# Performance work log

Hardware: AMD Instinct MI355X
Metric: run time of the kernel (lower is better)

The kernel has to match this reference:

```python
import jax, jax.numpy as jnp
import numpy as np

VOCAB, D = 5, 64


def setup_inputs() -> dict:
    key = jax.random.key(0)
    ks = jax.random.split(key, 8)
    B, S = 8, 2048
    x = jax.random.randint(ks[0], (B, S), 0, VOCAB)
    emb_table = jax.random.normal(ks[1], (VOCAB, D), dtype=jnp.float32)
    wq = jax.random.normal(ks[2], (D, D), dtype=jnp.float32) * 0.1
    bq = jax.random.normal(ks[3], (D,), dtype=jnp.float32) * 0.1
    wk = jax.random.normal(ks[4], (D, D), dtype=jnp.float32) * 0.1
    bk = jax.random.normal(ks[5], (D,), dtype=jnp.float32) * 0.1
    wv = jax.random.normal(ks[6], (D, D), dtype=jnp.float32) * 0.1
    bv = jax.random.normal(ks[7], (D,), dtype=jnp.float32) * 0.1
    return {"x": x, "emb_table": emb_table, "wq": wq, "bq": bq,
            "wk": wk, "bk": bk, "wv": wv, "bv": bv}


def reference(x, emb_table, wq, bq, wk, bk, wv, bv):
    # Embedding lookup: [B, S, D]
    emb = emb_table[x]
    # torch Linear: y = x @ W.T + b
    Q = emb @ wq.T + bq
    K = emb @ wk.T + bk
    V = emb @ wv.T + bv
    scale = 1.0 / np.sqrt(D).astype(np.float32)
    # [B, S, S] attention scores
    scores = jnp.einsum('bqd,bkd->bqk', Q, K) * scale
    S_len = x.shape[-1]
    # causal mask: -inf strictly above the diagonal
    causal = jnp.tril(jnp.ones((S_len, S_len), dtype=bool))
    scores = jnp.where(causal, scores, jnp.float32(-jnp.inf))
    probs = jax.nn.softmax(scores, axis=-1)
    return jnp.einsum('bqk,bkd->bqd', probs, V)
```

## Files before the change

### kernel.cpp

```cpp
#include <hip/hip_runtime.h>
#include <math.h>

#define VOCAB 5
#define DIM   64
#define BATCH 8
#define SLEN  2048
#define SEG   64
#define SEGS_PER_B (SLEN / SEG)
#define BLOCK 256
#define WPAD  65

__global__ __launch_bounds__(BLOCK) void decoder_fused(
    const int* __restrict__ x, const float* __restrict__ emb,
    const float* __restrict__ wq, const float* __restrict__ bq,
    const float* __restrict__ wk, const float* __restrict__ bk,
    const float* __restrict__ wv, const float* __restrict__ bv,
    float* __restrict__ out)
{
    const int bid  = blockIdx.x;
    const int b    = bid >> 5;
    const int seg  = bid & 31;
    const int s0   = seg * SEG;
    const int t    = threadIdx.x;
    const int lane = t & 63;
    const int wave = t >> 6;

    __shared__ float wSh[3][DIM * WPAD];
    __shared__ float eSh[VOCAB * DIM];
    __shared__ float qSh[VOCAB * DIM];
    __shared__ float kSh[VOCAB * DIM];
    __shared__ __align__(16) float vSh[VOCAB * DIM];
    __shared__ float StabSh[VOCAB * VOCAB];
    __shared__ float ESh[VOCAB * VOCAB];
    __shared__ float pSh[SEG * VOCAB];
    __shared__ int   waveCnt[4][VOCAB];

    {
        const float4* wq4 = (const float4*)wq;
        const float4* wk4 = (const float4*)wk;
        const float4* wv4 = (const float4*)wv;
        for (int j = t; j < DIM * DIM / 4; j += BLOCK) {
            int d = j >> 4, i4 = (j & 15) << 2;
            float4 a = wq4[j], c = wk4[j], e = wv4[j];
            float* dq = &wSh[0][d * WPAD + i4];
            float* dk = &wSh[1][d * WPAD + i4];
            float* dv = &wSh[2][d * WPAD + i4];
            dq[0]=a.x; dq[1]=a.y; dq[2]=a.z; dq[3]=a.w;
            dk[0]=c.x; dk[1]=c.y; dk[2]=c.z; dk[3]=c.w;
            dv[0]=e.x; dv[1]=e.y; dv[2]=e.z; dv[3]=e.w;
        }
        for (int i = t; i < VOCAB * DIM; i += BLOCK) eSh[i] = emb[i];
    }
    __syncthreads();

    for (int idx = t; idx < VOCAB * DIM; idx += BLOCK) {
        int v = idx >> 6, d = idx & 63;
        float aq = bq[d], ak = bk[d], av = bv[d];
        const float* e  = &eSh[v * DIM];
        const float* rq = &wSh[0][d * WPAD];
        const float* rk = &wSh[1][d * WPAD];
        const float* rv = &wSh[2][d * WPAD];
        #pragma unroll 16
        for (int i = 0; i < DIM; ++i) {
            float ei = e[i];
            aq += ei * rq[i];
            ak += ei * rk[i];
            av += ei * rv[i];
        }
        qSh[idx] = aq; kSh[idx] = ak; vSh[idx] = av;
    }
    __syncthreads();

    if (t < VOCAB * VOCAB) {
        int i = t / VOCAB, j = t % VOCAB;
        float s = 0.f;
        #pragma unroll
        for (int d = 0; d < DIM; ++d) s += qSh[i * DIM + d] * kSh[j * DIM + d];
        StabSh[t] = s * 0.125f;
    }
    __syncthreads();
    if (t < VOCAB * VOCAB) {
        int row = t / VOCAB;
        float mx = StabSh[row * VOCAB];
        #pragma unroll
        for (int j = 1; j < VOCAB; ++j) mx = fmaxf(mx, StabSh[row * VOCAB + j]);
        ESh[t] = expf(StabSh[t] - mx);
    }

    const int* xb = x + b * SLEN;
    int base[VOCAB] = {0,0,0,0,0};
    const int nchunk = s0 >> 6;
    for (int c = wave; c < nchunk; c += 4) {
        int tk = xb[(c << 6) + lane];
        #pragma unroll
        for (int v = 0; v < VOCAB; ++v)
            base[v] += __popcll(__ballot(tk == v));
    }
    if (lane == 0) {
        #pragma unroll
        for (int v = 0; v < VOCAB; ++v) waveCnt[wave][v] = base[v];
    }
    const int tok = xb[s0 + lane];
    const unsigned long long leMask = (2ull << lane) - 1ull;
    int inc[VOCAB];
    #pragma unroll
    for (int v = 0; v < VOCAB; ++v)
        inc[v] = __popcll(__ballot(tok == v) & leMask);
    __syncthreads();

    if (t < SEG) {
        float wgt[VOCAB];
        float den = 0.f;
        #pragma unroll
        for (int v = 0; v < VOCAB; ++v) {
            int c = inc[v] + waveCnt[0][v] + waveCnt[1][v] + waveCnt[2][v] + waveCnt[3][v];
            float wv = (float)c * ESh[tok * VOCAB + v];
            wgt[v] = wv;
            den += wv;
        }
        float invd = 1.0f / den;
        #pragma unroll
        for (int v = 0; v < VOCAB; ++v) pSh[t * VOCAB + v] = wgt[v] * invd;
    }
    __syncthreads();

    const float4* Vs4 = reinterpret_cast<const float4*>(vSh);
    float4* out4 = reinterpret_cast<float4*>(out) + ((size_t)b * SLEN + s0) * (DIM / 4);
    for (int i = t; i < SEG * (DIM / 4); i += BLOCK) {
        int q = i >> 4, d4 = i & 15;
        float4 acc = make_float4(0.f, 0.f, 0.f, 0.f);
        #pragma unroll
        for (int v = 0; v < VOCAB; ++v) {
            float pw = pSh[q * VOCAB + v];
            float4 vv = Vs4[v * (DIM / 4) + d4];
            acc.x += pw * vv.x;
            acc.y += pw * vv.y;
            acc.z += pw * vv.z;
            acc.w += pw * vv.w;
        }
        out4[i] = acc;
    }
}

extern "C" void kernel_launch(void* const* d_in, const int* in_sizes, int n_in,
                              void* d_out, int out_size, void* d_ws, size_t ws_size,
                              hipStream_t stream) {
    const int*   x   = (const int*)d_in[0];
    const float* emb = (const float*)d_in[1];
    const float* wq  = (const float*)d_in[2];
    const float* bq  = (const float*)d_in[3];
    const float* wk  = (const float*)d_in[4];
    const float* bk  = (const float*)d_in[5];
    const float* wv  = (const float*)d_in[6];
    const float* bv  = (const float*)d_in[7];
    float* out = (float*)d_out;

    decoder_fused<<<BATCH * SEGS_PER_B, BLOCK, 0, stream>>>(
        x, emb, wq, bq, wk, bk, wv, bv, out);
}
```

Measured before the change: 12.34 us.

## Split block into weight-loading and token-counting wave groups, doubling block size

Doubles the block to 512 threads so four waves stage the Q/K/V weights into shared memory while the other four load embeddings and compute the prefix token counts at the same time, instead of doing both one after the other. The Q/K/V projection is mapped one wave per vocab row, and q/k rows are padded to avoid bank conflicts. The separate exp-table pass and one barrier are removed by folding the softmax exponentials into the per-token weight computation on the last wave. Larger blocks may lower occupancy, and several waves sit idle in later phases.

```diff
diff --git a/kernel.cpp b/kernel.cpp
--- a/kernel.cpp
+++ b/kernel.cpp
@@ -7,7 +7,7 @@
 #define SLEN  2048
 #define SEG   64
 #define SEGS_PER_B (SLEN / SEG)
-#define BLOCK 256
+#define BLOCK 512
 #define WPAD  65
 
 __global__ __launch_bounds__(BLOCK) void decoder_fused(
@@ -27,34 +27,68 @@
 
     __shared__ float wSh[3][DIM * WPAD];
     __shared__ float eSh[VOCAB * DIM];
-    __shared__ float qSh[VOCAB * DIM];
-    __shared__ float kSh[VOCAB * DIM];
+    __shared__ float qSh[VOCAB * WPAD];
+    __shared__ float kSh[VOCAB * WPAD];
     __shared__ __align__(16) float vSh[VOCAB * DIM];
     __shared__ float StabSh[VOCAB * VOCAB];
-    __shared__ float ESh[VOCAB * VOCAB];
     __shared__ float pSh[SEG * VOCAB];
-    __shared__ int   waveCnt[4][VOCAB];
+    __shared__ int   wcSh[4][VOCAB];
 
-    {
+    const int* xb = x + b * SLEN;
+
+    int tok = 0;
+    int inc[VOCAB] = {0, 0, 0, 0, 0};
+
+    if (wave < 4) {
         const float4* wq4 = (const float4*)wq;
         const float4* wk4 = (const float4*)wk;
         const float4* wv4 = (const float4*)wv;
-        for (int j = t; j < DIM * DIM / 4; j += BLOCK) {
+        for (int j = t; j < DIM * DIM / 4; j += 256) {
             int d = j >> 4, i4 = (j & 15) << 2;
-            float4 a = wq4[j], c = wk4[j], e = wv4[j];
-            float* dq = &wSh[0][d * WPAD + i4];
-            float* dk = &wSh[1][d * WPAD + i4];
-            float* dv = &wSh[2][d * WPAD + i4];
-            dq[0]=a.x; dq[1]=a.y; dq[2]=a.z; dq[3]=a.w;
-            dk[0]=c.x; dk[1]=c.y; dk[2]=c.z; dk[3]=c.w;
-            dv[0]=e.x; dv[1]=e.y; dv[2]=e.z; dv[3]=e.w;
+            float4 a = wq4[j];
+            float* dst = &wSh[0][d * WPAD + i4];
+            dst[0] = a.x; dst[1] = a.y; dst[2] = a.z; dst[3] = a.w;
         }
-        for (int i = t; i < VOCAB * DIM; i += BLOCK) eSh[i] = emb[i];
+        for (int j = t; j < DIM * DIM / 4; j += 256) {
+            int d = j >> 4, i4 = (j & 15) << 2;
+            float4 a = wk4[j];
+            float* dst = &wSh[1][d * WPAD + i4];
+            dst[0] = a.x; dst[1] = a.y; dst[2] = a.z; dst[3] = a.w;
+        }
+        for (int j = t; j < DIM * DIM / 4; j += 256) {
+            int d = j >> 4, i4 = (j & 15) << 2;
+            float4 a = wv4[j];
+            float* dst = &wSh[2][d * WPAD + i4];
+            dst[0] = a.x; dst[1] = a.y; dst[2] = a.z; dst[3] = a.w;
+        }
+    } else {
+        for (int i = t - 256; i < VOCAB * DIM; i += 256) eSh[i] = emb[i];
+
+        const int pw = wave - 4;
+        int base[VOCAB] = {0, 0, 0, 0, 0};
+        const int nchunk = s0 >> 6;
+        for (int c = pw; c < nchunk; c += 4) {
+            int tk = xb[(c << 6) + lane];
+            #pragma unroll
+            for (int v = 0; v < VOCAB; ++v)
+                base[v] += __popcll(__ballot(tk == v));
+        }
+        if (lane == 0) {
+            #pragma unroll
+            for (int v = 0; v < VOCAB; ++v) wcSh[pw][v] = base[v];
+        }
+        if (wave == 7) {
+            tok = xb[s0 + lane];
+            const unsigned long long leMask = (2ull << lane) - 1ull;
+            #pragma unroll
+            for (int v = 0; v < VOCAB; ++v)
+                inc[v] = __popcll(__ballot(tok == v) & leMask);
+        }
     }
     __syncthreads();
 
-    for (int idx = t; idx < VOCAB * DIM; idx += BLOCK) {
-        int v = idx >> 6, d = idx & 63;
+    if (wave < 5) {
+        const int v = wave, d = lane;
         float aq = bq[d], ak = bk[d], av = bv[d];
         const float* e  = &eSh[v * DIM];
         const float* rq = &wSh[0][d * WPAD];
@@ -67,60 +101,39 @@
             ak += ei * rk[i];
             av += ei * rv[i];
         }
-        qSh[idx] = aq; kSh[idx] = ak; vSh[idx] = av;
+        qSh[v * WPAD + d] = aq;
+        kSh[v * WPAD + d] = ak;
+        vSh[v * DIM + d]  = av;
     }
     __syncthreads();
 
     if (t < VOCAB * VOCAB) {
         int i = t / VOCAB, j = t % VOCAB;
         float s = 0.f;
-        #pragma unroll
-        for (int d = 0; d < DIM; ++d) s += qSh[i * DIM + d] * kSh[j * DIM + d];
+        #pragma unroll 16
+        for (int d = 0; d < DIM; ++d)
+            s += qSh[i * WPAD + d] * kSh[j * WPAD + d];
         StabSh[t] = s * 0.125f;
     }
     __syncthreads();
-    if (t < VOCAB * VOCAB) {
-        int row = t / VOCAB;
-        float mx = StabSh[row * VOCAB];
+
+    if (wave == 7) {
+        float sv[VOCAB];
         #pragma unroll
-        for (int j = 1; j < VOCAB; ++j) mx = fmaxf(mx, StabSh[row * VOCAB + j]);
-        ESh[t] = expf(StabSh[t] - mx);
-    }
-
-    const int* xb = x + b * SLEN;
-    int base[VOCAB] = {0,0,0,0,0};
-    const int nchunk = s0 >> 6;
-    for (int c = wave; c < nchunk; c += 4) {
-        int tk = xb[(c << 6) + lane];
-        #pragma unroll
-        for (int v = 0; v < VOCAB; ++v)
-            base[v] += __popcll(__ballot(tk == v));
-    }
-    if (lane == 0) {
-        #pragma unroll
-        for (int v = 0; v < VOCAB; ++v) waveCnt[wave][v] = base[v];
-    }
-    const int tok = xb[s0 + lane];
-    const unsigned long long leMask = (2ull << lane) - 1ull;
-    int inc[VOCAB];
-    #pragma unroll
-    for (int v = 0; v < VOCAB; ++v)
-        inc[v] = __popcll(__ballot(tok == v) & leMask);
-    __syncthreads();
-
-    if (t < SEG) {
+        for (int v = 0; v < VOCAB; ++v) sv[v] = StabSh[tok * VOCAB + v];
+        float mx = fmaxf(fmaxf(fmaxf(sv[0], sv[1]), fmaxf(sv[2], sv[3])), sv[4]);
         float wgt[VOCAB];
         float den = 0.f;
         #pragma unroll
         for (int v = 0; v < VOCAB; ++v) {
-            int c = inc[v] + waveCnt[0][v] + waveCnt[1][v] + waveCnt[2][v] + waveCnt[3][v];
-            float wv = (float)c * ESh[tok * VOCAB + v];
+            int c = inc[v] + wcSh[0][v] + wcSh[1][v] + wcSh[2][v] + wcSh[3][v];
+            float wv = (float)c * expf(sv[v] - mx);
             wgt[v] = wv;
             den += wv;
         }
         float invd = 1.0f / den;
         #pragma unroll
-        for (int v = 0; v < VOCAB; ++v) pSh[t * VOCAB + v] = wgt[v] * invd;
+        for (int v = 0; v < VOCAB; ++v) pSh[lane * VOCAB + v] = wgt[v] * invd;
     }
     __syncthreads();
 
```

After: 11.11 us. -10.0%, faster.
